# Kernel optimization log

Measured on AMD Instinct MI355X. Metric: run time of the kernel, lower is better.

The kernel has to match this reference:

```python
import jax, jax.numpy as jnp
import numpy as np

B, S, D = 2, 2048, 4096
H, ROT = 16, 64
HD = D // H  # 256


def rotate_every_two(x):
    # x: (..., d) with d even; interleave (-x_odd, x_even)
    x1 = x[..., ::2]
    x2 = x[..., 1::2]
    return jnp.stack((-x2, x1), axis=-1).reshape(x.shape)


def setup_inputs() -> dict:
    key = jax.random.key(0)
    ks = jax.random.split(key, 8)
    hidden_states = jax.random.normal(ks[0], (B, S, D), dtype=jnp.float32)
    # GPT-J style repeat-interleaved sin/cos over rotary_dim, broadcast over heads
    inv_freq = 1.0 / (10000.0 ** (jnp.arange(0, ROT, 2, dtype=jnp.float32) / ROT))
    t = jnp.arange(S, dtype=jnp.float32)
    freqs = jnp.einsum('s,f->sf', t, inv_freq)                    # (S, ROT/2)
    freqs = jnp.repeat(freqs, 2, axis=-1)                         # (S, ROT)
    sin = jnp.sin(freqs)[None, :, None, :]                        # (1, S, 1, ROT)
    cos = jnp.cos(freqs)[None, :, None, :]
    scale = 0.02
    Wq = jax.random.normal(ks[1], (D, D), dtype=jnp.float32) * scale
    Wk = jax.random.normal(ks[2], (D, D), dtype=jnp.float32) * scale
    Wv = jax.random.normal(ks[3], (D, D), dtype=jnp.float32) * scale
    Wo = jax.random.normal(ks[4], (D, D), dtype=jnp.float32) * scale
    return {"hidden_states": hidden_states, "sin": sin, "cos": cos,
            "Wq": Wq, "Wk": Wk, "Wv": Wv, "Wo": Wo}


def reference(hidden_states, sin, cos, Wq, Wk, Wv, Wo):
    b, s, d = hidden_states.shape
    # projections (nn.Linear, no bias): y = x @ W.T
    q = (hidden_states @ Wq.T).reshape(b, s, H, HD)
    k = (hidden_states @ Wk.T).reshape(b, s, H, HD)
    v = (hidden_states @ Wv.T).reshape(b, s, H, HD)

    def rope(x):
        x_rot, x_pass = x[..., :ROT], x[..., ROT:]
        x_rot = x_rot * cos + rotate_every_two(x_rot) * sin
        return jnp.concatenate([x_rot, x_pass], axis=-1)

    q = rope(q).transpose(0, 2, 1, 3)  # (B, H, S, HD)
    k = rope(k).transpose(0, 2, 1, 3)
    v = v.transpose(0, 2, 1, 3)

    inv_scale = 1.0 / np.sqrt(HD).astype(np.float32)
    scores = jnp.einsum('bhqd,bhkd->bhqk', q, k) * inv_scale      # (B, H, S, S)
    # scaled_masked_triangular_softmax == causal masked softmax
    causal = jnp.tril(jnp.ones((s, s), dtype=bool))
    scores = jnp.where(causal[None, None], scores, jnp.finfo(scores.dtype).min)
    attn = jax.nn.softmax(scores, axis=-1)
    out = jnp.einsum('bhqk,bhkd->bhqd', attn, v)                  # (B, H, S, HD)
    out = out.transpose(0, 2, 1, 3).reshape(b, s, d)              # merge heads
    return out @ Wo.T
```

## Files before the change

kernel.cpp:

```cpp
#include <hip/hip_runtime.h>
#include <cstdint>
#include <cstddef>

#define TB 2
#define TS 2048
#define TD 4096
#define TH 16
#define THD 256
#define TROT 64
#define TM (TB*TS)

typedef __attribute__((ext_vector_type(8))) short bf16x8;
typedef __attribute__((ext_vector_type(4))) float f32x4;

#define LGKM0  asm volatile("s_waitcnt lgkmcnt(0)" ::: "memory")
#define VMCNT8 asm volatile("s_waitcnt vmcnt(8)" ::: "memory")
#define VMCNT4 asm volatile("s_waitcnt vmcnt(4)" ::: "memory")
#define VMCNT0 asm volatile("s_waitcnt vmcnt(0)" ::: "memory")
#define SBAR   __builtin_amdgcn_s_barrier()
#define SCHED0 __builtin_amdgcn_sched_barrier(0)

__device__ __forceinline__ unsigned short f2bf(float f) {
  union { float f; unsigned u; } v; v.f = f;
  return (unsigned short)((v.u + 0x7fffu + ((v.u >> 16) & 1u)) >> 16);
}

__device__ __forceinline__ void gld16(const void* g, void* l) {
  __builtin_amdgcn_global_load_lds(
      (const __attribute__((address_space(1))) unsigned int*)g,
      (__attribute__((address_space(3))) unsigned int*)l, 16, 0, 0);
}

__global__ __launch_bounds__(256) void k_cvt5(
    const float* __restrict__ s0, const float* __restrict__ s1,
    const float* __restrict__ s2, const float* __restrict__ s3,
    const float* __restrict__ s4, unsigned short* __restrict__ dst) {
  int i = blockIdx.x * 256 + threadIdx.x;
  int tsel = i >> 22, il = i & 4194303;
  const float* s = tsel == 0 ? s0 : tsel == 1 ? s1 : tsel == 2 ? s2 : tsel == 3 ? s3 : s4;
  float4 v = reinterpret_cast<const float4*>(s)[il];
  ushort4 o;
  o.x = f2bf(v.x); o.y = f2bf(v.y); o.z = f2bf(v.z); o.w = f2bf(v.w);
  *reinterpret_cast<ushort4*>(dst + (size_t)i * 4) = o;
}

template<int MODE>
__global__ __launch_bounds__(512, 2) void k_gemm(
    const unsigned short* __restrict__ A, const unsigned short* __restrict__ W,
    void* __restrict__ out, const float* __restrict__ sinp, const float* __restrict__ cosp)
{
  __shared__ unsigned short lds[32768];
  const int K = TD;
  const int t = threadIdx.x;
  const int w = t >> 6, l = t & 63, lr = l & 15, lh = l >> 4;
  const int wr = w >> 2, wc = w & 3;

  const int id = blockIdx.x;
  const int swz = (id & 7) * 32 + (id >> 3);
  const int m0 = (swz >> 4) * 256, n0 = (swz & 15) * 256;

  const int llo = lr * 32 + ((lh ^ ((lr >> 1) & 3)) * 8);

  size_t offA[2], offB[2];
#pragma unroll
  for (int it = 0; it < 2; ++it) {
    int c = it * 512 + t;
    int row = (c >> 6) * 16 + ((c >> 2) & 15);
    int cch = (c & 3) ^ ((c >> 3) & 3);
    offA[it] = (size_t)(m0 + row) * K + cch * 8;
    offB[it] = (size_t)(n0 + row) * K + cch * 8;
  }

  f32x4 acc[8][4];
#pragma unroll
  for (int i = 0; i < 8; ++i)
#pragma unroll
    for (int j = 0; j < 4; ++j) acc[i][j] = 0.f;

  gld16(W + offB[0], &lds[8192 + t*8]);
  gld16(W + offB[1], &lds[8192 + (512+t)*8]);
  gld16(A + offA[0], &lds[t*8]);
  gld16(A + offA[1], &lds[(512+t)*8]);
  gld16(W + offB[0] + 32, &lds[16384 + 8192 + t*8]);
  gld16(W + offB[1] + 32, &lds[16384 + 8192 + (512+t)*8]);
  gld16(A + offA[0] + 32, &lds[16384 + t*8]);
  gld16(A + offA[1] + 32, &lds[16384 + (512+t)*8]);
  VMCNT4;
  SBAR;
  SCHED0;

  const int abase = wr * 8 * 512;
  const int bbase = 8192 + wc * 4 * 512;

  for (int i2 = 0; i2 < 64; ++i2) {
    const bool pf = (i2 < 63);
    const int ke2 = (i2 + 1) * 64;
    bf16x8 af[4], bfr[4];

#pragma unroll
    for (int n = 0; n < 4; ++n)  bfr[n] = *(const bf16x8*)&lds[bbase + n*512 + llo];
#pragma unroll
    for (int mi = 0; mi < 4; ++mi) af[mi] = *(const bf16x8*)&lds[abase + mi*512 + llo];
    LGKM0; SBAR; SCHED0;
    if (pf) {
      gld16(W + offB[0] + ke2, &lds[8192 + t*8]);
      gld16(W + offB[1] + ke2, &lds[8192 + (512+t)*8]);
    }
    __builtin_amdgcn_s_setprio(1);
#pragma unroll
    for (int mi = 0; mi < 4; ++mi)
#pragma unroll
      for (int n = 0; n < 4; ++n)
        acc[mi][n] = __builtin_amdgcn_mfma_f32_16x16x32_bf16(af[mi], bfr[n], acc[mi][n], 0,0,0);
    __builtin_amdgcn_s_setprio(0);
    SBAR;

#pragma unroll
    for (int mi = 0; mi < 4; ++mi) af[mi] = *(const bf16x8*)&lds[abase + (4+mi)*512 + llo];
    LGKM0; SBAR; SCHED0;
    if (pf) {
      gld16(A + offA[0] + ke2, &lds[t*8]);
      gld16(A + offA[1] + ke2, &lds[(512+t)*8]);
    }
    __builtin_amdgcn_s_setprio(1);
#pragma unroll
    for (int mi = 0; mi < 4; ++mi)
#pragma unroll
      for (int n = 0; n < 4; ++n)
        acc[4+mi][n] = __builtin_amdgcn_mfma_f32_16x16x32_bf16(af[mi], bfr[n], acc[4+mi][n], 0,0,0);
    __builtin_amdgcn_s_setprio(0);
    if (pf) { VMCNT4; } else { VMCNT0; }
    SBAR; SCHED0;

#pragma unroll
    for (int n = 0; n < 4; ++n)  bfr[n] = *(const bf16x8*)&lds[16384 + bbase + n*512 + llo];
#pragma unroll
    for (int mi = 0; mi < 4; ++mi) af[mi] = *(const bf16x8*)&lds[16384 + abase + mi*512 + llo];
    LGKM0; SBAR; SCHED0;
    if (pf) {
      gld16(W + offB[0] + ke2 + 32, &lds[16384 + 8192 + t*8]);
      gld16(W + offB[1] + ke2 + 32, &lds[16384 + 8192 + (512+t)*8]);
    }
    __builtin_amdgcn_s_setprio(1);
#pragma unroll
    for (int mi = 0; mi < 4; ++mi)
#pragma unroll
      for (int n = 0; n < 4; ++n)
        acc[mi][n] = __builtin_amdgcn_mfma_f32_16x16x32_bf16(af[mi], bfr[n], acc[mi][n], 0,0,0);
    __builtin_amdgcn_s_setprio(0);
    SBAR;

#pragma unroll
    for (int mi = 0; mi < 4; ++mi) af[mi] = *(const bf16x8*)&lds[16384 + abase + (4+mi)*512 + llo];
    LGKM0; SBAR; SCHED0;
    if (pf) {
      gld16(A + offA[0] + ke2 + 32, &lds[16384 + t*8]);
      gld16(A + offA[1] + ke2 + 32, &lds[16384 + (512+t)*8]);
    }
    __builtin_amdgcn_s_setprio(1);
#pragma unroll
    for (int mi = 0; mi < 4; ++mi)
#pragma unroll
      for (int n = 0; n < 4; ++n)
        acc[4+mi][n] = __builtin_amdgcn_mfma_f32_16x16x32_bf16(af[mi], bfr[n], acc[4+mi][n], 0,0,0);
    __builtin_amdgcn_s_setprio(0);
    if (pf) { VMCNT4; } else { VMCNT0; }
    SBAR; SCHED0;
  }

  if constexpr (MODE == 2) {
    const int b = m0 >> 11, sbase = m0 & (TS - 1);
#pragma unroll
    for (int p = 0; p < 4; ++p) {
      __syncthreads();
      if (wc == p) {
#pragma unroll
        for (int m = 0; m < 8; ++m)
#pragma unroll
          for (int n = 0; n < 4; ++n) {
            int lcol = n * 16 + lr;
            int srow = wr * 128 + m * 16 + lh * 4;
            ushort4 o;
            o.x = f2bf(acc[m][n][0]); o.y = f2bf(acc[m][n][1]);
            o.z = f2bf(acc[m][n][2]); o.w = f2bf(acc[m][n][3]);
            *(ushort4*)&lds[lcol * 280 + srow] = o;
          }
      }
      __syncthreads();
#pragma unroll
      for (int i = 0; i < 4; ++i) {
        int q = i * 512 + t;
        int dl = q >> 5, sc = q & 31;
        uint4 v = *(const uint4*)&lds[dl * 280 + sc * 8];
        int d = n0 + p * 64 + dl;
        *(uint4*)((unsigned short*)out +
                  ((size_t)((b * TH + (d >> 8)) * THD + (d & 255))) * TS + sbase + sc * 8) = v;
      }
    }
  } else {
#pragma unroll
    for (int m = 0; m < 8; ++m)
#pragma unroll
      for (int n = 0; n < 4; ++n)
#pragma unroll
        for (int r = 0; r < 4; ++r) {
          int row = m0 + wr * 128 + m * 16 + lh * 4 + r;
          int col = n0 + wc * 64 + n * 16 + lr;
          float x = acc[m][n][r];
          if constexpr (MODE == 0) {
            ((float*)out)[(size_t)row * TD + col] = x;
          } else {
            float part = __shfl_xor(x, 1, 64);
            int s = row & (TS - 1), b = row >> 11;
            int h = col >> 8, d = col & 255;
            float val = x;
            if (d < TROT) {
              float cc = cosp[s * TROT + d], ss = sinp[s * TROT + d];
              val = x * cc + ((d & 1) ? part : -part) * ss;
            }
            ((unsigned short*)out)[((size_t)(b * TH + h) * TS + s) * THD + d] = f2bf(val);
          }
        }
  }
}

__global__ __launch_bounds__(256, 2) void k_fattn(
    const unsigned short* __restrict__ Qt, const unsigned short* __restrict__ Kt,
    const unsigned short* __restrict__ Vt, unsigned short* __restrict__ O)
{
  extern __shared__ unsigned short sh[];
  const int t = threadIdx.x, w = t >> 6, l = t & 63, lr = l & 15, lh = l >> 4;
  const int bh = blockIdx.x;
  const int qb = (gridDim.y - 1) - blockIdx.y;
  const int q0 = qb * 64;
  const int jmax = qb;

  const unsigned short* kbase = Kt + (size_t)bh * TS * THD;
  const unsigned short* vbase = Vt + (size_t)bh * THD * TS;

  const int llo = lr * 32 + ((lh ^ ((lr >> 1) & 3)) * 8);

  int koff[8], voff[8];
#pragma unroll
  for (int it = 0; it < 8; ++it) {
    int c = it * 256 + t;
    int row = (c >> 2) & 15;
    int scc = (c & 3) ^ ((row >> 1) & 3);
    koff[it] = (((c >> 9) & 3) * 16 + row) * THD + ((c >> 6) & 7) * 32 + scc * 8;
    voff[it] = (((c >> 6) & 15) * 16 + row) * TS + ((c >> 10) & 1) * 32 + scc * 8;
  }

  bf16x8 qf[8];
  const unsigned short* qp = Qt + ((size_t)bh * TS + q0 + w * 16 + lr) * THD;
#pragma unroll
  for (int kk = 0; kk < 8; ++kk) qf[kk] = *(const bf16x8*)(qp + kk * 32 + lh * 8);

  f32x4 oacc[16];
#pragma unroll
  for (int i = 0; i < 16; ++i) oacc[i] = 0.f;
  float mrow[4] = {-__builtin_inff(), -__builtin_inff(), -__builtin_inff(), -__builtin_inff()};
  float lrow[4] = {0.f, 0.f, 0.f, 0.f};

#pragma unroll
  for (int it = 0; it < 8; ++it) gld16(kbase + koff[it], &sh[(it*256 + t) * 8]);
#pragma unroll
  for (int it = 0; it < 8; ++it) gld16(vbase + voff[it], &sh[16384 + (it*256 + t) * 8]);

  for (int j = 0; j <= jmax; ++j) {
    const bool nx = (j < jmax);
    VMCNT8; SBAR; SCHED0;

    f32x4 sacc[4];
#pragma unroll
    for (int nt = 0; nt < 4; ++nt) sacc[nt] = 0.f;
    __builtin_amdgcn_s_setprio(1);
#pragma unroll
    for (int nt = 0; nt < 4; ++nt)
#pragma unroll
      for (int kk = 0; kk < 8; ++kk) {
        bf16x8 kf = *(const bf16x8*)&sh[(nt*8 + kk)*512 + llo];
        sacc[nt] = __builtin_amdgcn_mfma_f32_16x16x32_bf16(qf[kk], kf, sacc[nt], 0, 0, 0);
      }
    __builtin_amdgcn_s_setprio(0);
    LGKM0; SBAR; SCHED0;
    if (nx) {
      const unsigned short* kj = kbase + (size_t)(j + 1) * 64 * THD;
#pragma unroll
      for (int it = 0; it < 8; ++it) gld16(kj + koff[it], &sh[(it*256 + t) * 8]);
    }

    float p[4][4], tmax[4];
    const int qrow0 = q0 + w * 16 + lh * 4;
#pragma unroll
    for (int r = 0; r < 4; ++r) tmax[r] = -__builtin_inff();
#pragma unroll
    for (int nt = 0; nt < 4; ++nt) {
      int kpos = j * 64 + nt * 16 + lr;
#pragma unroll
      for (int r = 0; r < 4; ++r) {
        float sv = sacc[nt][r] * 0.0625f;
        if (kpos > qrow0 + r) sv = -__builtin_inff();
        p[nt][r] = sv;
        tmax[r] = fmaxf(tmax[r], sv);
      }
    }
#pragma unroll
    for (int off = 1; off < 16; off <<= 1)
#pragma unroll
      for (int r = 0; r < 4; ++r) tmax[r] = fmaxf(tmax[r], __shfl_xor(tmax[r], off, 64));

    float g = fmaxf(fmaxf(tmax[0] - mrow[0], tmax[1] - mrow[1]),
                    fmaxf(tmax[2] - mrow[2], tmax[3] - mrow[3]));
    if (__any(g > 8.f)) {
      float alpha[4];
#pragma unroll
      for (int r = 0; r < 4; ++r) {
        float mn = fmaxf(mrow[r], tmax[r]);
        alpha[r] = __expf(mrow[r] - mn);
        mrow[r] = mn;
        lrow[r] *= alpha[r];
      }
#pragma unroll
      for (int i = 0; i < 16; ++i)
#pragma unroll
        for (int r = 0; r < 4; ++r) oacc[i][r] *= alpha[r];
    }

    float tsum[4] = {0.f, 0.f, 0.f, 0.f};
#pragma unroll
    for (int nt = 0; nt < 4; ++nt)
#pragma unroll
      for (int r = 0; r < 4; ++r) {
        float pe = __expf(p[nt][r] - mrow[r]);
        p[nt][r] = pe;
        tsum[r] += pe;
      }
#pragma unroll
    for (int off = 1; off < 16; off <<= 1)
#pragma unroll
      for (int r = 0; r < 4; ++r) tsum[r] += __shfl_xor(tsum[r], off, 64);
#pragma unroll
    for (int r = 0; r < 4; ++r) lrow[r] += tsum[r];

    const int wb = 32768 + w * 1152;
#pragma unroll
    for (int nt = 0; nt < 4; ++nt)
#pragma unroll
      for (int r = 0; r < 4; ++r)
        sh[wb + (lh*4 + r)*72 + nt*16 + lr] = f2bf(p[nt][r]);
    bf16x8 pfr0 = *(const bf16x8*)&sh[wb + lr*72 + lh*8];
    bf16x8 pfr1 = *(const bf16x8*)&sh[wb + lr*72 + 32 + lh*8];

    if (nx) { VMCNT8; } else { VMCNT0; }
    SBAR; SCHED0;
    __builtin_amdgcn_s_setprio(1);
#pragma unroll
    for (int dt = 0; dt < 16; ++dt) {
      bf16x8 vf = *(const bf16x8*)&sh[16384 + dt*512 + llo];
      oacc[dt] = __builtin_amdgcn_mfma_f32_16x16x32_bf16(pfr0, vf, oacc[dt], 0, 0, 0);
    }
#pragma unroll
    for (int dt = 0; dt < 16; ++dt) {
      bf16x8 vf = *(const bf16x8*)&sh[16384 + (16 + dt)*512 + llo];
      oacc[dt] = __builtin_amdgcn_mfma_f32_16x16x32_bf16(pfr1, vf, oacc[dt], 0, 0, 0);
    }
    __builtin_amdgcn_s_setprio(0);
    LGKM0; SBAR; SCHED0;
    if (nx) {
      const unsigned short* vj = vbase + (size_t)(j + 1) * 64;
#pragma unroll
      for (int it = 0; it < 8; ++it) gld16(vj + voff[it], &sh[16384 + (it*256 + t) * 8]);
    }
  }

  const int b = bh >> 4, h = bh & 15;
  float inv[4];
#pragma unroll
  for (int r = 0; r < 4; ++r) inv[r] = 1.f / lrow[r];
#pragma unroll
  for (int dt = 0; dt < 16; ++dt)
#pragma unroll
    for (int r = 0; r < 4; ++r) {
      int s = q0 + w * 16 + lh * 4 + r;
      O[((size_t)(b * TS + s) * TH + h) * THD + dt * 16 + lr] = f2bf(oacc[dt][r] * inv[r]);
    }
}

extern "C" void kernel_launch(void* const* d_in, const int* in_sizes, int n_in,
                              void* d_out, int out_size, void* d_ws, size_t ws_size,
                              hipStream_t stream) {
  const float* hs   = (const float*)d_in[0];
  const float* sinp = (const float*)d_in[1];
  const float* cosp = (const float*)d_in[2];
  const float* Wq   = (const float*)d_in[3];
  const float* Wk   = (const float*)d_in[4];
  const float* Wv   = (const float*)d_in[5];
  const float* Wo   = (const float*)d_in[6];

  const size_t NE = (size_t)TM * TD;
  const size_t BYTES = NE * 2;
  char* ws = (char*)d_ws;
  unsigned short* hsb = (unsigned short*)(ws + 0*BYTES);
  unsigned short* Wqb = (unsigned short*)(ws + 1*BYTES);
  unsigned short* Wkb = (unsigned short*)(ws + 2*BYTES);
  unsigned short* Wvb = (unsigned short*)(ws + 3*BYTES);
  unsigned short* Wob = (unsigned short*)(ws + 4*BYTES);
  unsigned short* Qt  = (unsigned short*)(ws + 5*BYTES);
  unsigned short* Ktb = (unsigned short*)(ws + 6*BYTES);
  unsigned short* Vtb = (unsigned short*)(ws + 7*BYTES);
  unsigned short* Ob  = (unsigned short*)(ws + 8*BYTES);

  k_cvt5<<<81920, 256, 0, stream>>>(hs, Wq, Wk, Wv, Wo, hsb);

  k_gemm<1><<<256, 512, 0, stream>>>(hsb, Wqb, (void*)Qt,  sinp, cosp);
  k_gemm<1><<<256, 512, 0, stream>>>(hsb, Wkb, (void*)Ktb, sinp, cosp);
  k_gemm<2><<<256, 512, 0, stream>>>(hsb, Wvb, (void*)Vtb, nullptr, nullptr);

  k_fattn<<<dim3(TB*TH, TS/64), 256, 74752, stream>>>(Qt, Ktb, Vtb, Ob);

  k_gemm<0><<<256, 512, 0, stream>>>(Ob, Wob, d_out, nullptr, nullptr);
}
```

Before: 817.5 us.

## Restructure GEMM into quadrant-phased 8-stage pipeline with 128KB LDS double buffering

Rewrites the 256x256 bf16 GEMM main loop so each step computes one 128x128 quadrant per phase, with a 64-wide K tile split into halves and loaded into a 128KB dynamic-LDS double buffer. Each phase issues one staged global-to-LDS copy and waits on finer vmcnt thresholds, so loads overlap compute over a deeper pipeline. The wave-to-tile mapping changes (wm/wn quadrant layout) and the V-transpose epilogue is adjusted to match. Occupancy drops to one block per CU because of the large LDS footprint, and the last iterations re-load a clamped tile redundantly.

New measurement: 757.3 us. 1.08x faster.

```diff
diff --git a/kernel.cpp b/kernel.cpp
--- a/kernel.cpp
+++ b/kernel.cpp
@@ -15,7 +15,6 @@
 
 #define LGKM0  asm volatile("s_waitcnt lgkmcnt(0)" ::: "memory")
 #define VMCNT8 asm volatile("s_waitcnt vmcnt(8)" ::: "memory")
-#define VMCNT4 asm volatile("s_waitcnt vmcnt(4)" ::: "memory")
 #define VMCNT0 asm volatile("s_waitcnt vmcnt(0)" ::: "memory")
 #define SBAR   __builtin_amdgcn_s_barrier()
 #define SCHED0 __builtin_amdgcn_sched_barrier(0)
@@ -45,15 +44,15 @@
 }
 
 template<int MODE>
-__global__ __launch_bounds__(512, 2) void k_gemm(
+__global__ __launch_bounds__(512, 1) void k_gemm(
     const unsigned short* __restrict__ A, const unsigned short* __restrict__ W,
     void* __restrict__ out, const float* __restrict__ sinp, const float* __restrict__ cosp)
 {
-  __shared__ unsigned short lds[32768];
+  extern __shared__ unsigned short lds[];
   const int K = TD;
   const int t = threadIdx.x;
   const int w = t >> 6, l = t & 63, lr = l & 15, lh = l >> 4;
-  const int wr = w >> 2, wc = w & 3;
+  const int wm = w >> 2, wn = w & 3;
 
   const int id = blockIdx.x;
   const int swz = (id & 7) * 32 + (id >> 3);
@@ -61,166 +60,139 @@
 
   const int llo = lr * 32 + ((lh ^ ((lr >> 1) & 3)) * 8);
 
-  size_t offA[2], offB[2];
+  const unsigned short* srcA = A + (size_t)m0 * K;
+  const unsigned short* srcB = W + (size_t)n0 * K;
+
+  int roff[2];
 #pragma unroll
   for (int it = 0; it < 2; ++it) {
     int c = it * 512 + t;
-    int row = (c >> 6) * 16 + ((c >> 2) & 15);
-    int cch = (c & 3) ^ ((c >> 3) & 3);
-    offA[it] = (size_t)(m0 + row) * K + cch * 8;
-    offB[it] = (size_t)(n0 + row) * K + cch * 8;
-  }
-
-  f32x4 acc[8][4];
-#pragma unroll
-  for (int i = 0; i < 8; ++i)
-#pragma unroll
-    for (int j = 0; j < 4; ++j) acc[i][j] = 0.f;
-
-  gld16(W + offB[0], &lds[8192 + t*8]);
-  gld16(W + offB[1], &lds[8192 + (512+t)*8]);
-  gld16(A + offA[0], &lds[t*8]);
-  gld16(A + offA[1], &lds[(512+t)*8]);
-  gld16(W + offB[0] + 32, &lds[16384 + 8192 + t*8]);
-  gld16(W + offB[1] + 32, &lds[16384 + 8192 + (512+t)*8]);
-  gld16(A + offA[0] + 32, &lds[16384 + t*8]);
-  gld16(A + offA[1] + 32, &lds[16384 + (512+t)*8]);
-  VMCNT4;
-  SBAR;
-  SCHED0;
-
-  const int abase = wr * 8 * 512;
-  const int bbase = 8192 + wc * 4 * 512;
-
-  for (int i2 = 0; i2 < 64; ++i2) {
-    const bool pf = (i2 < 63);
-    const int ke2 = (i2 + 1) * 64;
-    bf16x8 af[4], bfr[4];
-
-#pragma unroll
-    for (int n = 0; n < 4; ++n)  bfr[n] = *(const bf16x8*)&lds[bbase + n*512 + llo];
-#pragma unroll
-    for (int mi = 0; mi < 4; ++mi) af[mi] = *(const bf16x8*)&lds[abase + mi*512 + llo];
-    LGKM0; SBAR; SCHED0;
-    if (pf) {
-      gld16(W + offB[0] + ke2, &lds[8192 + t*8]);
-      gld16(W + offB[1] + ke2, &lds[8192 + (512+t)*8]);
-    }
-    __builtin_amdgcn_s_setprio(1);
-#pragma unroll
-    for (int mi = 0; mi < 4; ++mi)
-#pragma unroll
-      for (int n = 0; n < 4; ++n)
-        acc[mi][n] = __builtin_amdgcn_mfma_f32_16x16x32_bf16(af[mi], bfr[n], acc[mi][n], 0,0,0);
-    __builtin_amdgcn_s_setprio(0);
-    SBAR;
-
-#pragma unroll
-    for (int mi = 0; mi < 4; ++mi) af[mi] = *(const bf16x8*)&lds[abase + (4+mi)*512 + llo];
-    LGKM0; SBAR; SCHED0;
-    if (pf) {
-      gld16(A + offA[0] + ke2, &lds[t*8]);
-      gld16(A + offA[1] + ke2, &lds[(512+t)*8]);
-    }
-    __builtin_amdgcn_s_setprio(1);
-#pragma unroll
-    for (int mi = 0; mi < 4; ++mi)
-#pragma unroll
-      for (int n = 0; n < 4; ++n)
-        acc[4+mi][n] = __builtin_amdgcn_mfma_f32_16x16x32_bf16(af[mi], bfr[n], acc[4+mi][n], 0,0,0);
-    __builtin_amdgcn_s_setprio(0);
-    if (pf) { VMCNT4; } else { VMCNT0; }
-    SBAR; SCHED0;
-
-#pragma unroll
-    for (int n = 0; n < 4; ++n)  bfr[n] = *(const bf16x8*)&lds[16384 + bbase + n*512 + llo];
-#pragma unroll
-    for (int mi = 0; mi < 4; ++mi) af[mi] = *(const bf16x8*)&lds[16384 + abase + mi*512 + llo];
-    LGKM0; SBAR; SCHED0;
-    if (pf) {
-      gld16(W + offB[0] + ke2 + 32, &lds[16384 + 8192 + t*8]);
-      gld16(W + offB[1] + ke2 + 32, &lds[16384 + 8192 + (512+t)*8]);
-    }
-    __builtin_amdgcn_s_setprio(1);
-#pragma unroll
-    for (int mi = 0; mi < 4; ++mi)
-#pragma unroll
-      for (int n = 0; n < 4; ++n)
-        acc[mi][n] = __builtin_amdgcn_mfma_f32_16x16x32_bf16(af[mi], bfr[n], acc[mi][n], 0,0,0);
-    __builtin_amdgcn_s_setprio(0);
-    SBAR;
-
-#pragma unroll
-    for (int mi = 0; mi < 4; ++mi) af[mi] = *(const bf16x8*)&lds[16384 + abase + (4+mi)*512 + llo];
-    LGKM0; SBAR; SCHED0;
-    if (pf) {
-      gld16(A + offA[0] + ke2 + 32, &lds[16384 + t*8]);
-      gld16(A + offA[1] + ke2 + 32, &lds[16384 + (512+t)*8]);
-    }
-    __builtin_amdgcn_s_setprio(1);
-#pragma unroll
-    for (int mi = 0; mi < 4; ++mi)
-#pragma unroll
-      for (int n = 0; n < 4; ++n)
-        acc[4+mi][n] = __builtin_amdgcn_mfma_f32_16x16x32_bf16(af[mi], bfr[n], acc[4+mi][n], 0,0,0);
-    __builtin_amdgcn_s_setprio(0);
-    if (pf) { VMCNT4; } else { VMCNT0; }
-    SBAR; SCHED0;
-  }
+    int rl = (c >> 2) & 15;
+    roff[it] = (16 * (c >> 7) + rl) * K + ((c >> 6) & 1) * 32 + ((c & 3) ^ ((rl >> 1) & 3)) * 8;
+  }
+
+  f32x4 acc[2][2][4][2];
+#pragma unroll
+  for (int qa = 0; qa < 2; ++qa)
+#pragma unroll
+    for (int qb = 0; qb < 2; ++qb)
+#pragma unroll
+      for (int m = 0; m < 4; ++m)
+#pragma unroll
+        for (int n = 0; n < 2; ++n) acc[qa][qb][m][n] = 0.f;
+
+  bf16x8 af[4][2], bfv[2][2];
+
+#define STG(SBUF, SAB, SHALF, SKOFS) { \
+    const unsigned short* _s = (SAB) ? srcB : srcA; \
+    const int _b = (SBUF)*32768 + (SAB)*16384 + (SHALF)*8192; \
+    gld16(_s + (size_t)(SHALF)*128*TD + (SKOFS) + roff[0], &lds[_b + t*8]); \
+    gld16(_s + (size_t)(SHALF)*128*TD + (SKOFS) + roff[1], &lds[_b + (512+t)*8]); }
+
+#define PHASE(BUF, QA, QB, DOAF, SBUF, SAB, SHALF, SKOFS, VMN) { \
+    if (DOAF) { \
+      _Pragma("unroll") for (int m = 0; m < 4; ++m) \
+      _Pragma("unroll") for (int kk = 0; kk < 2; ++kk) \
+        af[m][kk] = *(const bf16x8*)&lds[(BUF)*32768 + (QA)*8192 + ((wm*4+m)*2+kk)*512 + llo]; \
+    } \
+    _Pragma("unroll") for (int n = 0; n < 2; ++n) \
+    _Pragma("unroll") for (int kk = 0; kk < 2; ++kk) \
+      bfv[n][kk] = *(const bf16x8*)&lds[(BUF)*32768 + 16384 + (QB)*8192 + ((wn*2+n)*2+kk)*512 + llo]; \
+    LGKM0; SBAR; SCHED0; \
+    STG(SBUF, SAB, SHALF, SKOFS); \
+    asm volatile("s_waitcnt vmcnt(" #VMN ")" ::: "memory"); \
+    __builtin_amdgcn_s_setprio(1); \
+    _Pragma("unroll") for (int m = 0; m < 4; ++m) \
+    _Pragma("unroll") for (int n = 0; n < 2; ++n) \
+    _Pragma("unroll") for (int kk = 0; kk < 2; ++kk) \
+      acc[QA][QB][m][n] = __builtin_amdgcn_mfma_f32_16x16x32_bf16(af[m][kk], bfv[n][kk], acc[QA][QB][m][n], 0,0,0); \
+    __builtin_amdgcn_s_setprio(0); \
+    SBAR; SCHED0; }
+
+  const int NT = K / 64;
+
+  STG(0,0,0, 0);  SCHED0;
+  STG(0,1,0, 0);  SCHED0;
+  STG(0,0,1, 0);  SCHED0;
+  STG(0,1,1, 0);  SCHED0;
+  STG(1,0,0, 64); SCHED0;
+  STG(1,1,0, 64); SCHED0;
+  VMCNT8; SBAR; SCHED0;
+
+  for (int i2 = 0; i2 < NT/2; ++i2) {
+    const int k1c = (2*i2+1) * 64;
+    const int k0n = (2*i2+2 < NT ? 2*i2+2 : NT-1) * 64;
+    const int k1n = (2*i2+3 < NT ? 2*i2+3 : NT-1) * 64;
+    PHASE(0, 0,0, 1,  1,0,1, k1c, 6);
+    PHASE(0, 0,1, 0,  1,1,1, k1c, 8);
+    PHASE(0, 1,0, 1,  0,0,0, k0n, 10);
+    PHASE(0, 1,1, 0,  0,1,0, k0n, 8);
+    PHASE(1, 0,0, 1,  0,0,1, k0n, 6);
+    PHASE(1, 0,1, 0,  0,1,1, k0n, 8);
+    PHASE(1, 1,0, 1,  1,0,0, k1n, 10);
+    PHASE(1, 1,1, 0,  1,1,0, k1n, 8);
+  }
+#undef PHASE
+#undef STG
 
   if constexpr (MODE == 2) {
+    VMCNT0; SBAR;
     const int b = m0 >> 11, sbase = m0 & (TS - 1);
 #pragma unroll
-    for (int p = 0; p < 4; ++p) {
-      __syncthreads();
-      if (wc == p) {
-#pragma unroll
-        for (int m = 0; m < 8; ++m)
-#pragma unroll
-          for (int n = 0; n < 4; ++n) {
-            int lcol = n * 16 + lr;
-            int srow = wr * 128 + m * 16 + lh * 4;
+    for (int qb = 0; qb < 2; ++qb)
+#pragma unroll
+      for (int n = 0; n < 2; ++n) {
+        __syncthreads();
+#pragma unroll
+        for (int qa = 0; qa < 2; ++qa)
+#pragma unroll
+          for (int m = 0; m < 4; ++m) {
+            int lcol = wn * 16 + lr;
+            int srow = qa * 128 + wm * 64 + m * 16 + lh * 4;
             ushort4 o;
-            o.x = f2bf(acc[m][n][0]); o.y = f2bf(acc[m][n][1]);
-            o.z = f2bf(acc[m][n][2]); o.w = f2bf(acc[m][n][3]);
-            *(ushort4*)&lds[lcol * 280 + srow] = o;
+            o.x = f2bf(acc[qa][qb][m][n][0]); o.y = f2bf(acc[qa][qb][m][n][1]);
+            o.z = f2bf(acc[qa][qb][m][n][2]); o.w = f2bf(acc[qa][qb][m][n][3]);
+            *(ushort4*)&lds[lcol * 268 + srow] = o;
           }
-      }
-      __syncthreads();
-#pragma unroll
-      for (int i = 0; i < 4; ++i) {
-        int q = i * 512 + t;
-        int dl = q >> 5, sc = q & 31;
-        uint4 v = *(const uint4*)&lds[dl * 280 + sc * 8];
-        int d = n0 + p * 64 + dl;
-        *(uint4*)((unsigned short*)out +
-                  ((size_t)((b * TH + (d >> 8)) * THD + (d & 255))) * TS + sbase + sc * 8) = v;
-      }
-    }
+        __syncthreads();
+#pragma unroll
+        for (int rr = 0; rr < 4; ++rr) {
+          int idx = rr * 512 + t;
+          int dl = idx >> 5, sc = (idx & 31) * 8;
+          uint4 v = *(const uint4*)&lds[dl * 268 + sc];
+          int d = n0 + qb * 128 + (dl >> 4) * 32 + n * 16 + (dl & 15);
+          *(uint4*)((unsigned short*)out +
+                    ((size_t)((b * TH + (d >> 8)) * THD + (d & 255))) * TS + sbase + sc) = v;
+        }
+      }
   } else {
 #pragma unroll
-    for (int m = 0; m < 8; ++m)
-#pragma unroll
-      for (int n = 0; n < 4; ++n)
-#pragma unroll
-        for (int r = 0; r < 4; ++r) {
-          int row = m0 + wr * 128 + m * 16 + lh * 4 + r;
-          int col = n0 + wc * 64 + n * 16 + lr;
-          float x = acc[m][n][r];
-          if constexpr (MODE == 0) {
-            ((float*)out)[(size_t)row * TD + col] = x;
-          } else {
-            float part = __shfl_xor(x, 1, 64);
-            int s = row & (TS - 1), b = row >> 11;
-            int h = col >> 8, d = col & 255;
-            float val = x;
-            if (d < TROT) {
-              float cc = cosp[s * TROT + d], ss = sinp[s * TROT + d];
-              val = x * cc + ((d & 1) ? part : -part) * ss;
+    for (int qa = 0; qa < 2; ++qa)
+#pragma unroll
+      for (int qb = 0; qb < 2; ++qb)
+#pragma unroll
+        for (int m = 0; m < 4; ++m)
+#pragma unroll
+          for (int n = 0; n < 2; ++n)
+#pragma unroll
+            for (int r = 0; r < 4; ++r) {
+              int row = m0 + qa * 128 + wm * 64 + m * 16 + lh * 4 + r;
+              int col = n0 + qb * 128 + wn * 32 + n * 16 + lr;
+              float x = acc[qa][qb][m][n][r];
+              if constexpr (MODE == 0) {
+                ((float*)out)[(size_t)row * TD + col] = x;
+              } else {
+                float part = __shfl_xor(x, 1, 64);
+                int s = row & (TS - 1), b = row >> 11;
+                int h = col >> 8, d = col & 255;
+                float val = x;
+                if (d < TROT) {
+                  float cc = cosp[s * TROT + d], ss = sinp[s * TROT + d];
+                  val = x * cc + ((d & 1) ? part : -part) * ss;
+                }
+                ((unsigned short*)out)[((size_t)(b * TH + h) * TS + s) * THD + d] = f2bf(val);
+              }
             }
-            ((unsigned short*)out)[((size_t)(b * TH + h) * TS + s) * THD + d] = f2bf(val);
-          }
-        }
   }
 }
 
@@ -412,11 +384,11 @@
 
   k_cvt5<<<81920, 256, 0, stream>>>(hs, Wq, Wk, Wv, Wo, hsb);
 
-  k_gemm<1><<<256, 512, 0, stream>>>(hsb, Wqb, (void*)Qt,  sinp, cosp);
-  k_gemm<1><<<256, 512, 0, stream>>>(hsb, Wkb, (void*)Ktb, sinp, cosp);
-  k_gemm<2><<<256, 512, 0, stream>>>(hsb, Wvb, (void*)Vtb, nullptr, nullptr);
+  k_gemm<1><<<256, 512, 131072, stream>>>(hsb, Wqb, (void*)Qt,  sinp, cosp);
+  k_gemm<1><<<256, 512, 131072, stream>>>(hsb, Wkb, (void*)Ktb, sinp, cosp);
+  k_gemm<2><<<256, 512, 131072, stream>>>(hsb, Wvb, (void*)Vtb, nullptr, nullptr);
 
   k_fattn<<<dim3(TB*TH, TS/64), 256, 74752, stream>>>(Qt, Ktb, Vtb, Ob);
 
-  k_gemm<0><<<256, 512, 0, stream>>>(Ob, Wob, d_out, nullptr, nullptr);
-}
+  k_gemm<0><<<256, 512, 131072, stream>>>(Ob, Wob, d_out, nullptr, nullptr);
+}
```
